# Optimization experiments

Measured on AMD Instinct MI355X. Metric: run time of the kernel, lower is better.

Reference implementation:

```python
import jax, jax.numpy as jnp
import numpy as np

B, N, D, C = 256, 5, 2048, 1000   # batch, nodeNum, inputDim, num_classes
H = 1024                          # GCN hidden dim (dim_hid)
PROTO_M = 0.999                   # args.proto_m EMA momentum
EPS = 1e-12


def normalize_adj(a):
    # symmetric normalization D^-1/2 A D^-1/2 of the all-ones adjacency
    d = jnp.sum(a, axis=1)
    dinv = 1.0 / jnp.sqrt(d)
    return a * dinv[:, None] * dinv[None, :]


def setup_inputs() -> dict:
    key = jax.random.key(0)
    ks = jax.random.split(key, 8)
    x = jax.random.normal(ks[0], (B, N, D), jnp.float32)          # region features (post-backbone)
    target = jax.random.randint(ks[1], (B,), 0, C)                # labels
    prototypes = jax.random.normal(ks[2], (C, N, D), jnp.float32)  # prototype memory bank
    adj = normalize_adj(jnp.ones((N, N), jnp.float32))            # adjMatrix_q
    s = 0.02
    W1 = jax.random.normal(ks[3], (D, H), jnp.float32) * s        # GCN layer 1
    W2 = jax.random.normal(ks[4], (H, D), jnp.float32) * s        # GCN layer 2
    Wg = jax.random.normal(ks[5], (N * D, D), jnp.float32) * s    # fc_g
    bg = jnp.zeros((D,), jnp.float32)
    Wc = jax.random.normal(ks[6], (D, C), jnp.float32) * s        # fc_cls
    bc = jnp.zeros((C,), jnp.float32)
    return dict(x=x, target=target, prototypes=prototypes, adj=adj,
                W1=W1, W2=W2, Wg=Wg, bg=bg, Wc=Wc, bc=bc)


def reference(x, target, prototypes, adj, W1, W2, Wg, bg, Wc, bc):
    # --- Res_Gcn (non-proto path): 2-layer GCN over the N region nodes ---
    h = jax.nn.relu(jnp.einsum('nm,bmd,dh->bnh', adj, x, W1))      # [B,N,H]
    nodes = jnp.einsum('nm,bmh,hd->bnd', adj, h, W2)               # [B,N,D]
    g = nodes.reshape(B, N * D) @ Wg + bg                          # fc_g -> [B,D]
    pred = g @ Wc + bc                                             # fc_cls -> [B,C]

    # --- sequential per-sample EMA scatter-update of prototype bank ---
    # order matters for duplicate labels, so use lax.scan (sequential)
    def step(protos, inp):
        feat, label = inp                                          # feat: [N,D]
        new = protos[label] * PROTO_M + (1.0 - PROTO_M) * feat
        return protos.at[label].set(new), None

    protos, _ = jax.lax.scan(step, prototypes, (x, target))

    # F.normalize(prototypes, p=2, dim=1): L2 norm over the node axis
    norm = jnp.sqrt(jnp.sum(protos * protos, axis=1, keepdims=True))
    protos = protos / jnp.maximum(norm, EPS)
    return pred, protos
```

## Files before the change

kernel.cpp:

```cpp
#include <hip/hip_runtime.h>
#include <hip/hip_bf16.h>
#include <math.h>

#define BB 256
#define NN 5
#define DD 2048
#define CC 1000
#define HH 1024
#define PROTO_M 0.999f

typedef unsigned short u16;
typedef __attribute__((ext_vector_type(8))) short short8;
typedef __attribute__((ext_vector_type(4))) float f32x4;

__device__ __forceinline__ u16 f2bf(float f) {
    union { float f; unsigned u; } x; x.f = f;
    unsigned r = x.u + 0x7fff + ((x.u >> 16) & 1);
    return (u16)(r >> 16);
}
__device__ __forceinline__ float bf2f(u16 b) {
    union { unsigned u; float f; } x; x.u = ((unsigned)b) << 16;
    return x.f;
}

__global__ __launch_bounds__(256) void transpose_bf16(const float* __restrict__ in,
                                                      u16* __restrict__ out,
                                                      int K, int N) {
    constexpr int STR = 72;
    __shared__ u16 T[64 * STR];
    const int k0 = blockIdx.x * 64, n0 = blockIdx.y * 64;
    const int t = threadIdx.x;
    const int c4 = t % 16;
    const int rr = t / 16;
#pragma unroll
    for (int p = 0; p < 4; ++p) {
        int k = p * 16 + rr;
        int n = c4 * 4;
        if (n0 + n < N) {
            float4 v = *(const float4*)(in + (size_t)(k0 + k) * N + n0 + n);
            T[(n + 0) * STR + k] = f2bf(v.x);
            T[(n + 1) * STR + k] = f2bf(v.y);
            T[(n + 2) * STR + k] = f2bf(v.z);
            T[(n + 3) * STR + k] = f2bf(v.w);
        }
    }
    __syncthreads();
    const int ch = t % 8;
    const int nl0 = t / 8;
#pragma unroll
    for (int q = 0; q < 2; ++q) {
        int nl = nl0 + q * 32;
        if (n0 + nl < N) {
            short8 v = *(const short8*)(&T[nl * STR + ch * 8]);
            *(short8*)(out + (size_t)(n0 + nl) * K + k0 + ch * 8) = v;
        }
    }
}

template<bool IN_BF16>
__global__ __launch_bounds__(256) void adj_mix(const float* __restrict__ adjp,
                                               const void* __restrict__ X,
                                               u16* __restrict__ Y, int Dd) {
    __shared__ float as_[NN * NN];
    if (threadIdx.x < NN * NN) as_[threadIdx.x] = adjp[threadIdx.x];
    __syncthreads();
    const int d4n = Dd / 4;
    int idx = blockIdx.x * blockDim.x + threadIdx.x;
    int b = idx / d4n, d4 = idx % d4n;
    float xv[NN][4];
#pragma unroll
    for (int m = 0; m < NN; ++m) {
        size_t base = ((size_t)b * NN + m) * Dd + d4 * 4;
        if (IN_BF16) {
            const ushort4 u = *(const ushort4*)((const u16*)X + base);
            xv[m][0] = bf2f(u.x); xv[m][1] = bf2f(u.y);
            xv[m][2] = bf2f(u.z); xv[m][3] = bf2f(u.w);
        } else {
            const float4 f = *(const float4*)((const float*)X + base);
            xv[m][0] = f.x; xv[m][1] = f.y; xv[m][2] = f.z; xv[m][3] = f.w;
        }
    }
#pragma unroll
    for (int n = 0; n < NN; ++n) {
        float s[4] = {0.f, 0.f, 0.f, 0.f};
#pragma unroll
        for (int m = 0; m < NN; ++m) {
            float a = as_[n * NN + m];
#pragma unroll
            for (int j = 0; j < 4; ++j) s[j] += a * xv[m][j];
        }
        ushort4 o;
        o.x = f2bf(s[0]); o.y = f2bf(s[1]); o.z = f2bf(s[2]); o.w = f2bf(s[3]);
        *(ushort4*)(Y + ((size_t)b * NN + n) * Dd + d4 * 4) = o;
    }
}

template<int BM, int BN, bool ATOMIC, bool RELU>
__global__ __launch_bounds__(256) void gemm_mfma(const u16* __restrict__ A,
                                                 const u16* __restrict__ Bt,
                                                 void* __restrict__ C,
                                                 int M, int N, int K, int Ks) {
    constexpr int FM = BM / 32;
    constexpr int FN = BN / 32;
    constexpr int PA = BM / 64;
    constexpr int PB = BN / 64;
    __shared__ u16 As[2 * BM * 32];
    __shared__ u16 Bs[2 * BN * 32];
    const int t = threadIdx.x;
    const int lane = t & 63;
    const int wave = t >> 6;
    const int wr = wave >> 1, wc = wave & 1;
    const int lr = lane & 15;
    const int kc = lane >> 4;
    const int m0 = blockIdx.y * BM;
    const int n0 = blockIdx.x * BN;
    const int kz0 = blockIdx.z * Ks;
    const int srow = t >> 2;
    const int sc = t & 3;

    f32x4 acc[FM][FN];
#pragma unroll
    for (int i = 0; i < FM; ++i)
#pragma unroll
        for (int j = 0; j < FN; ++j) acc[i][j] = (f32x4){0.f, 0.f, 0.f, 0.f};

    const short8 zero8 = {0, 0, 0, 0, 0, 0, 0, 0};
    short8 ra[PA], rb[PB];

    auto LOAD = [&](int k0) {
#pragma unroll
        for (int p = 0; p < PA; ++p) {
            int row = p * 64 + srow;
            ra[p] = *(const short8*)(A + (size_t)(m0 + row) * K + k0 + sc * 8);
        }
#pragma unroll
        for (int p = 0; p < PB; ++p) {
            int row = p * 64 + srow;
            rb[p] = (n0 + row < N)
                ? *(const short8*)(Bt + (size_t)(n0 + row) * K + k0 + sc * 8)
                : zero8;
        }
    };
    auto WRITE = [&](int buf) {
#pragma unroll
        for (int p = 0; p < PA; ++p) {
            int row = p * 64 + srow;
            int ch = sc ^ ((row >> 1) & 3);
            *(short8*)(&As[buf * BM * 32 + row * 32 + ch * 8]) = ra[p];
        }
#pragma unroll
        for (int p = 0; p < PB; ++p) {
            int row = p * 64 + srow;
            int ch = sc ^ ((row >> 1) & 3);
            *(short8*)(&Bs[buf * BN * 32 + row * 32 + ch * 8]) = rb[p];
        }
    };

    const int nt = Ks / 32;
    LOAD(kz0);
    WRITE(0);
    for (int tt = 0; tt < nt; ++tt) {
        if (tt + 1 < nt) LOAD(kz0 + (tt + 1) * 32);
        __syncthreads();
        const int buf = tt & 1;
        short8 af[FM], bfr[FN];
#pragma unroll
        for (int i = 0; i < FM; ++i) {
            int row = wr * (BM / 2) + i * 16 + lr;
            int ch = kc ^ ((row >> 1) & 3);
            af[i] = *(const short8*)(&As[buf * BM * 32 + row * 32 + ch * 8]);
        }
#pragma unroll
        for (int j = 0; j < FN; ++j) {
            int row = wc * (BN / 2) + j * 16 + lr;
            int ch = kc ^ ((row >> 1) & 3);
            bfr[j] = *(const short8*)(&Bs[buf * BN * 32 + row * 32 + ch * 8]);
        }
#pragma unroll
        for (int i = 0; i < FM; ++i)
#pragma unroll
            for (int j = 0; j < FN; ++j)
                acc[i][j] = __builtin_amdgcn_mfma_f32_16x16x32_bf16(
                    af[i], bfr[j], acc[i][j], 0, 0, 0);
        __syncthreads();
        if (tt + 1 < nt) WRITE((tt + 1) & 1);
    }

#pragma unroll
    for (int i = 0; i < FM; ++i) {
        int row = m0 + wr * (BM / 2) + i * 16 + kc * 4;
#pragma unroll
        for (int j = 0; j < FN; ++j) {
            int col = n0 + wc * (BN / 2) + j * 16 + lr;
            if (col >= N) continue;
#pragma unroll
            for (int q = 0; q < 4; ++q) {
                float v = acc[i][j][q];
                if (ATOMIC) {
                    atomicAdd((float*)C + (size_t)(row + q) * N + col, v);
                } else {
                    if (RELU) v = fmaxf(v, 0.f);
                    ((u16*)C)[(size_t)(row + q) * N + col] = f2bf(v);
                }
            }
        }
    }
}

__global__ __launch_bounds__(256) void finalize_g(const float* __restrict__ gf,
                                                  const float* __restrict__ bg,
                                                  u16* __restrict__ gb) {
    int idx = blockIdx.x * blockDim.x + threadIdx.x;
    int n4 = idx % (DD / 4);
    float4 v = *(const float4*)(gf + (size_t)idx * 4);
    float4 b = *(const float4*)(bg + n4 * 4);
    ushort4 o;
    o.x = f2bf(v.x + b.x); o.y = f2bf(v.y + b.y);
    o.z = f2bf(v.z + b.z); o.w = f2bf(v.w + b.w);
    *(ushort4*)(gb + (size_t)idx * 4) = o;
}

__global__ __launch_bounds__(256) void finalize_pred(const float* __restrict__ pf,
                                                     const float* __restrict__ bc,
                                                     float* __restrict__ out) {
    int idx = blockIdx.x * blockDim.x + threadIdx.x;
    int n4 = idx % 250;
    float4 v = *(const float4*)(pf + (size_t)idx * 4);
    float4 b = *(const float4*)(bc + n4 * 4);
    float4 o; o.x = v.x + b.x; o.y = v.y + b.y; o.z = v.z + b.z; o.w = v.w + b.w;
    *(float4*)(out + (size_t)idx * 4) = o;
}

__global__ __launch_bounds__(1024) void rank_build(const int* __restrict__ target,
                                                   int* __restrict__ cnt,
                                                   int* __restrict__ start,
                                                   int* __restrict__ order,
                                                   float* __restrict__ coef,
                                                   float* __restrict__ decayc) {
    __shared__ int stgt[BB];
    __shared__ int scnt[1024];
    __shared__ int sscan[1024];
    const int t = threadIdx.x;
    scnt[t] = 0;
    if (t < BB) stgt[t] = target[t];
    __syncthreads();
    int myc = -1, posc = 0;
    if (t < BB) {
        myc = stgt[t];
        for (int b2 = 0; b2 < t; ++b2) posc += (stgt[b2] == myc) ? 1 : 0;
        atomicAdd(&scnt[myc], 1);
    }
    __syncthreads();
    sscan[t] = scnt[t];
    __syncthreads();
    for (int off = 1; off < 1024; off <<= 1) {
        int add = (t >= off) ? sscan[t - off] : 0;
        __syncthreads();
        sscan[t] += add;
        __syncthreads();
    }
    if (t < CC) {
        cnt[t] = scnt[t];
        start[t] = sscan[t] - scnt[t];
        decayc[t] = powf(PROTO_M, (float)scnt[t]);
    }
    __syncthreads();
    if (t < BB) {
        int s = sscan[myc] - scnt[myc];
        order[s + posc] = t;
        coef[s + posc] = (1.0f - PROTO_M) * powf(PROTO_M, (float)(scnt[myc] - 1 - posc));
    }
}

__global__ __launch_bounds__(256) void proto_fused(const float* __restrict__ protos,
                                                   const float* __restrict__ x,
                                                   const int* __restrict__ cnt,
                                                   const int* __restrict__ start,
                                                   const int* __restrict__ order,
                                                   const float* __restrict__ coef,
                                                   const float* __restrict__ decayc,
                                                   float* __restrict__ out) {
    const int c = blockIdx.x >> 1;
    const int d = ((blockIdx.x & 1) * 256 + threadIdx.x) * 4;
    const float dec = decayc[c];
    const int k = cnt[c];
    const int s = start[c];
    float4 v[NN];
#pragma unroll
    for (int n = 0; n < NN; ++n) {
        float4 p = *(const float4*)(protos + ((size_t)c * NN + n) * DD + d);
        v[n].x = p.x * dec; v[n].y = p.y * dec; v[n].z = p.z * dec; v[n].w = p.w * dec;
    }
    for (int j = 0; j < k; ++j) {
        int b = order[s + j];
        float cf = coef[s + j];
#pragma unroll
        for (int n = 0; n < NN; ++n) {
            float4 xv = *(const float4*)(x + ((size_t)b * NN + n) * DD + d);
            v[n].x += cf * xv.x; v[n].y += cf * xv.y;
            v[n].z += cf * xv.z; v[n].w += cf * xv.w;
        }
    }
    float ss[4] = {0.f, 0.f, 0.f, 0.f};
#pragma unroll
    for (int n = 0; n < NN; ++n) {
        ss[0] += v[n].x * v[n].x; ss[1] += v[n].y * v[n].y;
        ss[2] += v[n].z * v[n].z; ss[3] += v[n].w * v[n].w;
    }
    float inv[4];
#pragma unroll
    for (int j = 0; j < 4; ++j) inv[j] = 1.0f / fmaxf(sqrtf(ss[j]), 1e-12f);
#pragma unroll
    for (int n = 0; n < NN; ++n) {
        float4 o;
        o.x = v[n].x * inv[0]; o.y = v[n].y * inv[1];
        o.z = v[n].z * inv[2]; o.w = v[n].w * inv[3];
        *(float4*)(out + ((size_t)c * NN + n) * DD + d) = o;
    }
}

extern "C" void kernel_launch(void* const* d_in, const int* in_sizes, int n_in,
                              void* d_out, int out_size, void* d_ws, size_t ws_size,
                              hipStream_t stream) {
    const float* x          = (const float*)d_in[0];
    const int*   target     = (const int*)d_in[1];
    const float* prototypes = (const float*)d_in[2];
    const float* adj        = (const float*)d_in[3];
    const float* W1         = (const float*)d_in[4];
    const float* W2         = (const float*)d_in[5];
    const float* Wg         = (const float*)d_in[6];
    const float* bg         = (const float*)d_in[7];
    const float* Wc         = (const float*)d_in[8];
    const float* bc         = (const float*)d_in[9];

    float* out_pred   = (float*)d_out;
    float* out_protos = (float*)d_out + (size_t)BB * CC;

    char* w = (char*)d_ws;
    u16* Wgt     = (u16*)w;                 w += (size_t)DD * NN * DD * 2;
    u16* Wt      = (u16*)w;                 w += (size_t)DD * HH * 2 * 2;
    u16* ax      = (u16*)w;                 w += (size_t)BB * NN * DD * 2;
    u16* nodes   = ax;
    u16* h       = (u16*)w;                 w += (size_t)BB * NN * HH * 2;
    u16* ah      = (u16*)w;                 w += (size_t)BB * NN * HH * 2;
    float* g_f32 = (float*)w;               w += (size_t)BB * DD * 4;
    u16* g_bf16  = (u16*)w;                 w += (size_t)BB * DD * 2;
    float* pred_f32 = (float*)w;            w += (size_t)BB * CC * 4;
    int* cnt     = (int*)w;                 w += 1024 * 4;
    int* start   = (int*)w;                 w += 1024 * 4;
    int* order   = (int*)w;                 w += 256 * 4;
    float* coef  = (float*)w;               w += 256 * 4;
    float* decayc= (float*)w;               w += 1024 * 4;

    transpose_bf16<<<dim3(DD / 64, HH / 64), 256, 0, stream>>>(W1, Wt, DD, HH);
    adj_mix<false><<<(BB * DD / 4) / 256, 256, 0, stream>>>(adj, x, ax, DD);
    gemm_mfma<64, 64, false, true><<<dim3(HH / 64, (BB * NN) / 64, 1), 256, 0, stream>>>(
        ax, Wt, h, BB * NN, HH, DD, DD);
    adj_mix<true><<<(BB * HH / 4) / 256, 256, 0, stream>>>(adj, h, ah, HH);
    transpose_bf16<<<dim3(HH / 64, DD / 64), 256, 0, stream>>>(W2, Wt, HH, DD);
    gemm_mfma<64, 64, false, false><<<dim3(DD / 64, (BB * NN) / 64, 1), 256, 0, stream>>>(
        ah, Wt, nodes, BB * NN, DD, HH, HH);
    transpose_bf16<<<dim3((NN * DD) / 64, DD / 64), 256, 0, stream>>>(Wg, Wgt, NN * DD, DD);
    hipMemsetAsync(g_f32, 0, (size_t)BB * DD * 4, stream);
    gemm_mfma<128, 128, true, false><<<dim3(DD / 128, BB / 128, 8), 256, 0, stream>>>(
        nodes, Wgt, g_f32, BB, DD, NN * DD, NN * DD / 8);
    finalize_g<<<(BB * DD / 4) / 256, 256, 0, stream>>>(g_f32, bg, g_bf16);
    transpose_bf16<<<dim3(DD / 64, (CC + 63) / 64), 256, 0, stream>>>(Wc, Wt, DD, CC);
    hipMemsetAsync(pred_f32, 0, (size_t)BB * CC * 4, stream);
    gemm_mfma<128, 64, true, false><<<dim3((CC + 63) / 64, BB / 128, 8), 256, 0, stream>>>(
        g_bf16, Wt, pred_f32, BB, CC, DD, DD / 8);
    finalize_pred<<<(BB * 250) / 256, 256, 0, stream>>>(pred_f32, bc, out_pred);

    rank_build<<<1, 1024, 0, stream>>>(target, cnt, start, order, coef, decayc);
    proto_fused<<<CC * 2, 256, 0, stream>>>(prototypes, x, cnt, start, order,
                                            coef, decayc, out_protos);
}
```

Before: 338.2 us.

## Use direct global-to-LDS loads in GEMMs and retune split-K tiling

Replaces the register-staged, double-buffered GEMM with one that issues global_load_lds straight into an XOR-swizzled shared tile with BK=64, dropping the register round-trip. The first GEMM now uses split-K with fp32 atomics, and its ReLU moves into the following adj_mix. Tile sizes and split counts change for all GEMMs, and the weight transpose zero-pads to 1024 columns so the B loads need no bounds check. The separate memsets are merged into one. The new loop is single-buffered with two barriers per step, so load latency is no longer overlapped with MFMA work, and the extra atomics add traffic.

```diff
diff --git a/kernel.cpp b/kernel.cpp
--- a/kernel.cpp
+++ b/kernel.cpp
@@ -21,6 +21,12 @@
 __device__ __forceinline__ float bf2f(u16 b) {
     union { unsigned u; float f; } x; x.u = ((unsigned)b) << 16;
     return x.f;
+}
+
+__device__ __forceinline__ void gload16(const u16* g, u16* l) {
+    __builtin_amdgcn_global_load_lds(
+        (const __attribute__((address_space(1))) unsigned int*)g,
+        (__attribute__((address_space(3))) unsigned int*)l, 16, 0, 0);
 }
 
 __global__ __launch_bounds__(256) void transpose_bf16(const float* __restrict__ in,
@@ -47,17 +53,17 @@
     __syncthreads();
     const int ch = t % 8;
     const int nl0 = t / 8;
+    const short8 zero8 = {0, 0, 0, 0, 0, 0, 0, 0};
 #pragma unroll
     for (int q = 0; q < 2; ++q) {
         int nl = nl0 + q * 32;
-        if (n0 + nl < N) {
-            short8 v = *(const short8*)(&T[nl * STR + ch * 8]);
-            *(short8*)(out + (size_t)(n0 + nl) * K + k0 + ch * 8) = v;
-        }
-    }
-}
-
-template<bool IN_BF16>
+        short8 v = zero8;
+        if (n0 + nl < N) v = *(const short8*)(&T[nl * STR + ch * 8]);
+        *(short8*)(out + (size_t)(n0 + nl) * K + k0 + ch * 8) = v;
+    }
+}
+
+template<bool IN_BF16, bool RELU_IN>
 __global__ __launch_bounds__(256) void adj_mix(const float* __restrict__ adjp,
                                                const void* __restrict__ X,
                                                u16* __restrict__ Y, int Dd) {
@@ -79,6 +85,10 @@
             const float4 f = *(const float4*)((const float*)X + base);
             xv[m][0] = f.x; xv[m][1] = f.y; xv[m][2] = f.z; xv[m][3] = f.w;
         }
+        if (RELU_IN) {
+#pragma unroll
+            for (int j = 0; j < 4; ++j) xv[m][j] = fmaxf(xv[m][j], 0.f);
+        }
     }
 #pragma unroll
     for (int n = 0; n < NN; ++n) {
@@ -96,27 +106,27 @@
 }
 
 template<int BM, int BN, bool ATOMIC, bool RELU>
-__global__ __launch_bounds__(256) void gemm_mfma(const u16* __restrict__ A,
-                                                 const u16* __restrict__ Bt,
-                                                 void* __restrict__ C,
-                                                 int M, int N, int K, int Ks) {
+__global__ __launch_bounds__(256) void gemm_gl(const u16* __restrict__ A,
+                                               const u16* __restrict__ Bt,
+                                               void* __restrict__ C,
+                                               int M, int N, int K, int Ks) {
     constexpr int FM = BM / 32;
     constexpr int FN = BN / 32;
-    constexpr int PA = BM / 64;
-    constexpr int PB = BN / 64;
-    __shared__ u16 As[2 * BM * 32];
-    __shared__ u16 Bs[2 * BN * 32];
+    constexpr int SEGA = BM / 32;
+    constexpr int SEGB = BN / 32;
+    __shared__ u16 As[BM * 64];
+    __shared__ u16 Bs[BN * 64];
     const int t = threadIdx.x;
     const int lane = t & 63;
-    const int wave = t >> 6;
-    const int wr = wave >> 1, wc = wave & 1;
+    const int w = t >> 6;
+    const int wr = w >> 1, wc = w & 1;
     const int lr = lane & 15;
     const int kc = lane >> 4;
+    const int lrow8 = lane >> 3;
+    const int lc = lane & 7;
     const int m0 = blockIdx.y * BM;
     const int n0 = blockIdx.x * BN;
     const int kz0 = blockIdx.z * Ks;
-    const int srow = t >> 2;
-    const int sc = t & 3;
 
     f32x4 acc[FM][FN];
 #pragma unroll
@@ -124,66 +134,46 @@
 #pragma unroll
         for (int j = 0; j < FN; ++j) acc[i][j] = (f32x4){0.f, 0.f, 0.f, 0.f};
 
-    const short8 zero8 = {0, 0, 0, 0, 0, 0, 0, 0};
-    short8 ra[PA], rb[PB];
-
-    auto LOAD = [&](int k0) {
-#pragma unroll
-        for (int p = 0; p < PA; ++p) {
-            int row = p * 64 + srow;
-            ra[p] = *(const short8*)(A + (size_t)(m0 + row) * K + k0 + sc * 8);
-        }
-#pragma unroll
-        for (int p = 0; p < PB; ++p) {
-            int row = p * 64 + srow;
-            rb[p] = (n0 + row < N)
-                ? *(const short8*)(Bt + (size_t)(n0 + row) * K + k0 + sc * 8)
-                : zero8;
-        }
-    };
-    auto WRITE = [&](int buf) {
-#pragma unroll
-        for (int p = 0; p < PA; ++p) {
-            int row = p * 64 + srow;
-            int ch = sc ^ ((row >> 1) & 3);
-            *(short8*)(&As[buf * BM * 32 + row * 32 + ch * 8]) = ra[p];
-        }
-#pragma unroll
-        for (int p = 0; p < PB; ++p) {
-            int row = p * 64 + srow;
-            int ch = sc ^ ((row >> 1) & 3);
-            *(short8*)(&Bs[buf * BN * 32 + row * 32 + ch * 8]) = rb[p];
-        }
-    };
-
-    const int nt = Ks / 32;
-    LOAD(kz0);
-    WRITE(0);
-    for (int tt = 0; tt < nt; ++tt) {
-        if (tt + 1 < nt) LOAD(kz0 + (tt + 1) * 32);
+    for (int k0 = kz0; k0 < kz0 + Ks; k0 += 64) {
         __syncthreads();
-        const int buf = tt & 1;
-        short8 af[FM], bfr[FN];
-#pragma unroll
-        for (int i = 0; i < FM; ++i) {
-            int row = wr * (BM / 2) + i * 16 + lr;
-            int ch = kc ^ ((row >> 1) & 3);
-            af[i] = *(const short8*)(&As[buf * BM * 32 + row * 32 + ch * 8]);
-        }
-#pragma unroll
-        for (int j = 0; j < FN; ++j) {
-            int row = wc * (BN / 2) + j * 16 + lr;
-            int ch = kc ^ ((row >> 1) & 3);
-            bfr[j] = *(const short8*)(&Bs[buf * BN * 32 + row * 32 + ch * 8]);
-        }
-#pragma unroll
-        for (int i = 0; i < FM; ++i)
-#pragma unroll
-            for (int j = 0; j < FN; ++j)
-                acc[i][j] = __builtin_amdgcn_mfma_f32_16x16x32_bf16(
-                    af[i], bfr[j], acc[i][j], 0, 0, 0);
+#pragma unroll
+        for (int p = 0; p < SEGA; ++p) {
+            int s = p * 4 + w;
+            int r = s * 8 + lrow8;
+            int cs = lc ^ (r & 7);
+            gload16(A + (size_t)(m0 + r) * K + k0 + cs * 8, &As[s * 512]);
+        }
+#pragma unroll
+        for (int p = 0; p < SEGB; ++p) {
+            int s = p * 4 + w;
+            int r = s * 8 + lrow8;
+            int cs = lc ^ (r & 7);
+            gload16(Bt + (size_t)(n0 + r) * K + k0 + cs * 8, &Bs[s * 512]);
+        }
         __syncthreads();
-        if (tt + 1 < nt) WRITE((tt + 1) & 1);
+
+#pragma unroll
+        for (int ks = 0; ks < 2; ++ks) {
+            short8 af[FM], bfr[FN];
+#pragma unroll
+            for (int i = 0; i < FM; ++i) {
+                int row = wr * (BM / 2) + i * 16 + lr;
+                int cs = (ks * 4 + kc) ^ (row & 7);
+                af[i] = *(const short8*)(&As[row * 64 + cs * 8]);
+            }
+#pragma unroll
+            for (int j = 0; j < FN; ++j) {
+                int row = wc * (BN / 2) + j * 16 + lr;
+                int cs = (ks * 4 + kc) ^ (row & 7);
+                bfr[j] = *(const short8*)(&Bs[row * 64 + cs * 8]);
+            }
+#pragma unroll
+            for (int i = 0; i < FM; ++i)
+#pragma unroll
+                for (int j = 0; j < FN; ++j)
+                    acc[i][j] = __builtin_amdgcn_mfma_f32_16x16x32_bf16(
+                        af[i], bfr[j], acc[i][j], 0, 0, 0);
+        }
     }
 
 #pragma unroll
@@ -337,37 +327,38 @@
     float* out_protos = (float*)d_out + (size_t)BB * CC;
 
     char* w = (char*)d_ws;
-    u16* Wgt     = (u16*)w;                 w += (size_t)DD * NN * DD * 2;
-    u16* Wt      = (u16*)w;                 w += (size_t)DD * HH * 2 * 2;
-    u16* ax      = (u16*)w;                 w += (size_t)BB * NN * DD * 2;
+    u16* Wgt     = (u16*)w;        w += (size_t)DD * NN * DD * 2;
+    u16* Wt      = (u16*)w;        w += (size_t)1024 * 2048 * 2 + 256;
+    u16* ax      = (u16*)w;        w += (size_t)BB * NN * DD * 2;
     u16* nodes   = ax;
-    u16* h       = (u16*)w;                 w += (size_t)BB * NN * HH * 2;
-    u16* ah      = (u16*)w;                 w += (size_t)BB * NN * HH * 2;
-    float* g_f32 = (float*)w;               w += (size_t)BB * DD * 4;
-    u16* g_bf16  = (u16*)w;                 w += (size_t)BB * DD * 2;
-    float* pred_f32 = (float*)w;            w += (size_t)BB * CC * 4;
-    int* cnt     = (int*)w;                 w += 1024 * 4;
-    int* start   = (int*)w;                 w += 1024 * 4;
-    int* order   = (int*)w;                 w += 256 * 4;
-    float* coef  = (float*)w;               w += 256 * 4;
-    float* decayc= (float*)w;               w += 1024 * 4;
+    u16* ah      = (u16*)w;        w += (size_t)BB * NN * HH * 2;
+    float* g1_f32   = (float*)w;   w += (size_t)BB * NN * HH * 4;
+    float* g_f32    = (float*)w;   w += (size_t)BB * DD * 4;
+    float* pred_f32 = (float*)w;   w += (size_t)BB * CC * 4;
+    char*  zero_end = w;
+    u16* g_bf16  = (u16*)w;        w += (size_t)BB * DD * 2;
+    int* cnt     = (int*)w;        w += 1024 * 4;
+    int* start   = (int*)w;        w += 1024 * 4;
+    int* order   = (int*)w;        w += 256 * 4;
+    float* coef  = (float*)w;      w += 256 * 4;
+    float* decayc= (float*)w;      w += 1024 * 4;
+
+    hipMemsetAsync(g1_f32, 0, (size_t)(zero_end - (char*)g1_f32), stream);
 
     transpose_bf16<<<dim3(DD / 64, HH / 64), 256, 0, stream>>>(W1, Wt, DD, HH);
-    adj_mix<false><<<(BB * DD / 4) / 256, 256, 0, stream>>>(adj, x, ax, DD);
-    gemm_mfma<64, 64, false, true><<<dim3(HH / 64, (BB * NN) / 64, 1), 256, 0, stream>>>(
-        ax, Wt, h, BB * NN, HH, DD, DD);
-    adj_mix<true><<<(BB * HH / 4) / 256, 256, 0, stream>>>(adj, h, ah, HH);
+    adj_mix<false, false><<<(BB * DD / 4) / 256, 256, 0, stream>>>(adj, x, ax, DD);
+    gemm_gl<128, 64, true, false><<<dim3(HH / 64, (BB * NN) / 128, 2), 256, 0, stream>>>(
+        ax, Wt, g1_f32, BB * NN, HH, DD, DD / 2);
+    adj_mix<false, true><<<(BB * HH / 4) / 256, 256, 0, stream>>>(adj, g1_f32, ah, HH);
     transpose_bf16<<<dim3(HH / 64, DD / 64), 256, 0, stream>>>(W2, Wt, HH, DD);
-    gemm_mfma<64, 64, false, false><<<dim3(DD / 64, (BB * NN) / 64, 1), 256, 0, stream>>>(
+    gemm_gl<128, 64, false, false><<<dim3(DD / 64, (BB * NN) / 128, 1), 256, 0, stream>>>(
         ah, Wt, nodes, BB * NN, DD, HH, HH);
     transpose_bf16<<<dim3((NN * DD) / 64, DD / 64), 256, 0, stream>>>(Wg, Wgt, NN * DD, DD);
-    hipMemsetAsync(g_f32, 0, (size_t)BB * DD * 4, stream);
-    gemm_mfma<128, 128, true, false><<<dim3(DD / 128, BB / 128, 8), 256, 0, stream>>>(
-        nodes, Wgt, g_f32, BB, DD, NN * DD, NN * DD / 8);
+    gemm_gl<128, 128, true, false><<<dim3(DD / 128, BB / 128, 16), 256, 0, stream>>>(
+        nodes, Wgt, g_f32, BB, DD, NN * DD, NN * DD / 16);
     finalize_g<<<(BB * DD / 4) / 256, 256, 0, stream>>>(g_f32, bg, g_bf16);
-    transpose_bf16<<<dim3(DD / 64, (CC + 63) / 64), 256, 0, stream>>>(Wc, Wt, DD, CC);
-    hipMemsetAsync(pred_f32, 0, (size_t)BB * CC * 4, stream);
-    gemm_mfma<128, 64, true, false><<<dim3((CC + 63) / 64, BB / 128, 8), 256, 0, stream>>>(
+    transpose_bf16<<<dim3(DD / 64, 16), 256, 0, stream>>>(Wc, Wt, DD, CC);
+    gemm_gl<128, 64, true, false><<<dim3(16, BB / 128, 8), 256, 0, stream>>>(
         g_bf16, Wt, pred_f32, BB, CC, DD, DD / 8);
     finalize_pred<<<(BB * 250) / 256, 256, 0, stream>>>(pred_f32, bc, out_pred);
 
```

Result: no change. 342.3 us (+1.2%).
